# Optimization experiments

Measured on AMD Instinct MI355X. Metric: run time of the kernel, lower is better.

Reference implementation:

```python
import jax, jax.numpy as jnp
import numpy as np

N, DIN, H, OUT = 2048, 128, 64, 7


def setup_inputs() -> dict:
    key = jax.random.key(0)
    ks = jax.random.split(key, 24)

    def lin(k, out_d, in_d):
        kw, kb = jax.random.split(k)
        s = 1.0 / np.sqrt(in_d)
        W = jax.random.uniform(kw, (out_d, in_d), minval=-s, maxval=s, dtype=jnp.float32)
        b = jax.random.uniform(kb, (out_d,), minval=-s, maxval=s, dtype=jnp.float32)
        return W, b

    x = jax.random.normal(ks[0], (N, DIN), dtype=jnp.float32)
    A = jax.random.uniform(ks[1], (N, N), dtype=jnp.float32)
    W1, b1 = lin(ks[2], H, DIN)
    WF1, bF1 = lin(ks[3], H, H)
    WF2, bF2 = lin(ks[4], H, H)
    WT1, bT1 = lin(ks[5], H, H)
    WT2, bT2 = lin(ks[6], H, H)
    WC1, bC1 = lin(ks[7], H, H)
    WC2, bC2 = lin(ks[8], H, H)
    Wa, ba = lin(ks[9], H, H)
    q = jax.random.normal(ks[10], (H,), dtype=jnp.float32)
    W2, b2 = lin(ks[11], OUT, H)
    return dict(x=x, A=A, k=4, W1=W1, b1=b1, WF1=WF1, bF1=bF1, WF2=WF2, bF2=bF2,
                WT1=WT1, bT1=bT1, WT2=WT2, bT2=bT2, WC1=WC1, bC1=bC1, WC2=WC2,
                bC2=bC2, Wa=Wa, ba=ba, q=q, W2=W2, b2=b2)


def leaky(x):
    return jnp.where(x > 0, x, 0.1 * x)


def laplacian(A):
    # D^{-1/2} A D^{-1/2} with diagonal D of (rowsum + 1e-10)
    d = (jnp.sum(A, -1) + 1e-10) ** -0.5
    return A * d[:, None] * d[None, :]


def cos_sim(x):
    n = jnp.sqrt(jnp.sum(x * x, -1, keepdims=True))
    s = x / n + 1e-10  # note: +1e-10 AFTER the division, as in the source
    return s @ s.T


def heat(x):
    # exp(-0.5 * sum_d ((x_i - x_j)^2 + 1e-10)); gram trick, same math as
    # the [d, N, N] broadcasted version in the source.
    sq = jnp.sum(x * x, -1)
    dist = sq[:, None] + sq[None, :] - 2.0 * (x @ x.T) + x.shape[-1] * 1e-10
    return jnp.exp(-0.5 * dist)


def l2_norm_rows(x):
    m = jnp.sqrt(jnp.mean(x * x, -1)) + 1e-10
    return x / m[:, None]


def hsic(x1, x2):
    n = x1.shape[-2]
    K1 = x1 @ x1.T
    K2 = x2 @ x2.T
    Rm = jnp.eye(n, dtype=x1.dtype) - jnp.ones((n, n), dtype=x1.dtype) / n
    P = Rm @ K1 @ Rm  # [N, N]
    # mean(I * (P @ K2)) * n^2/(n-1)^2 = trace(P @ K2)/(n-1)^2; K2 symmetric
    return jnp.sum(P * K2) / (n - 1) ** 2


def gnn(z, Ad, W, b):
    return leaky((Ad @ z) @ W.T + b)


def reference(x, A, k, W1, b1, WF1, bF1, WF2, bF2, WT1, bT1, WT2, bT2,
              WC1, bC1, WC2, bC2, Wa, ba, q, W2, b2):
    h = leaky(x @ W1.T + b1)                       # [N, H]
    At = laplacian(A)
    Hh = heat(h)                                    # [N, N]
    rank = jnp.argsort(jnp.argsort(-Hh, axis=-1), axis=-1)  # double-argsort rank
    mask = (rank < k).astype(h.dtype)
    Af = laplacian(cos_sim(h) * mask)
    zf = gnn(gnn(h, Af, WF1, bF1), Af, WF2, bF2)
    zt = gnn(gnn(h, At, WT1, bT1), At, WT2, bT2)
    zcf = gnn(gnn(h, Af, WC1, bC1), Af, WC2, bC2)
    zct = gnn(gnn(h, At, WC1, bC1), At, WC2, bC2)
    Lcf = l2_norm_rows(zcf)
    Lct = l2_norm_rows(zct)
    Lc = jnp.mean((Lcf @ Lcf.T - Lct @ Lct.T) ** 2)
    Ld = hsic(zt, zct) + hsic(zf, zcf)
    zc = (zcf + zct) / 2
    z = jnp.stack([zf, zt, zc], axis=-2)            # [N, 3, H]
    a = jax.nn.softmax(jnp.tanh(z @ Wa.T + ba) @ q, axis=-1)  # [N, 3]
    zagg = jnp.einsum('nkd,nk->nd', z, a)           # [N, H]
    out = zagg @ W2.T + b2                          # [N, OUT]
    return (out, Lc, Ld)
```

## Files before the change

kernel.cpp:

```cpp
#include <hip/hip_runtime.h>
#include <stdint.h>

#define N 2048
#define DIN 128
#define H 64
#define OUTD 7
#define RS 32
#define S1 8
#define S2 8

#define Z_ZT  0
#define Z_ZCT 64
#define Z_ZF  128
#define Z_ZCF 192
#define Z_LCF 256
#define Z_LCT 320

typedef short bf16x8 __attribute__((ext_vector_type(8)));
typedef float floatx4 __attribute__((ext_vector_type(4)));

__device__ __forceinline__ float leaky(float x){ return x > 0.f ? x : 0.1f*x; }

__device__ __forceinline__ unsigned short f2bf(float f){
  unsigned int u = __float_as_uint(f);
  u = u + 0x7FFFu + ((u >> 16) & 1u);
  return (unsigned short)(u >> 16);
}

__device__ __forceinline__ float bf2f(unsigned short u){
  return __uint_as_float((unsigned int)u << 16);
}

__device__ __forceinline__ float waveRedSum(float v){
  #pragma unroll
  for (int o = 32; o > 0; o >>= 1) v += __shfl_xor(v, o, 64);
  return v;
}

__device__ __forceinline__ unsigned long long shflx64(unsigned long long v, int m){
  unsigned int lo = (unsigned int)v, hi = (unsigned int)(v >> 32);
  lo = (unsigned int)__shfl_xor((int)lo, m, 64);
  hi = (unsigned int)__shfl_xor((int)hi, m, 64);
  return ((unsigned long long)hi << 32) | lo;
}

__global__ void k_prep(const float* __restrict__ A, float* __restrict__ dA,
                       unsigned short* __restrict__ Abf){
  int i = blockIdx.x;
  const float4* row = (const float4*)(A + (size_t)i * N);
  unsigned short* ob = Abf + (size_t)i * N;
  float s = 0.f;
  #pragma unroll
  for (int it = 0; it < 2; it++){
    int u = threadIdx.x + it*256;
    float4 v = row[u];
    s += v.x + v.y + v.z + v.w;
    ushort4 o;
    o.x = f2bf(v.x); o.y = f2bf(v.y); o.z = f2bf(v.z); o.w = f2bf(v.w);
    *(ushort4*)&ob[u*4] = o;
  }
  __shared__ float red[4];
  s = waveRedSum(s);
  int wid = threadIdx.x >> 6, lane = threadIdx.x & 63;
  if (lane == 0) red[wid] = s;
  __syncthreads();
  if (threadIdx.x == 0){
    float t = red[0] + red[1] + red[2] + red[3];
    dA[i] = 1.0f / sqrtf(t + 1e-10f);
  }
}

__global__ __launch_bounds__(256) void k_h(const float* __restrict__ x,
                    const float* __restrict__ W1g, const float* __restrict__ b1,
                    const float* __restrict__ dA,
                    unsigned short* __restrict__ hb_hi,
                    unsigned short* __restrict__ hb_lo,
                    unsigned short* __restrict__ hsT,
                    float* __restrict__ sq, float* __restrict__ hsum){
  __shared__ float W1t[DIN][H+1];
  __shared__ float xb[4][DIN];
  __shared__ __align__(16) unsigned short hTb[H][16];
  int tid = threadIdx.x, w = tid >> 6, t = tid & 63;
  int i0 = blockIdx.x * 16;
  for (int u = tid; u < 2048; u += 256){
    float4 g = ((const float4*)W1g)[u];
    int row = u >> 5, c0 = (u & 31) * 4;
    W1t[c0+0][row] = g.x; W1t[c0+1][row] = g.y;
    W1t[c0+2][row] = g.z; W1t[c0+3][row] = g.w;
  }
  __syncthreads();
  float bt = b1[t];
  for (int rr = 0; rr < 4; rr++){
    int i = i0 + w*4 + rr;
    xb[w][t]      = x[(size_t)i*DIN + t];
    xb[w][t + 64] = x[(size_t)i*DIN + t + 64];
    float acc = bt;
    #pragma unroll
    for (int c4 = 0; c4 < DIN/4; c4++){
      float xv[4]; *(float4*)xv = *(const float4*)&xb[w][c4*4];
      acc += xv[0]*W1t[c4*4+0][t] + xv[1]*W1t[c4*4+1][t]
           + xv[2]*W1t[c4*4+2][t] + xv[3]*W1t[c4*4+3][t];
    }
    float hv = leaky(acc);
    unsigned short hi = f2bf(hv);
    hb_hi[(size_t)i*H + t] = hi;
    hb_lo[(size_t)i*H + t] = f2bf(hv - bf2f(hi));
    hTb[t][w*4+rr] = f2bf(dA[i]*hv);
    float s2 = waveRedSum(hv*hv);
    float s1 = waveRedSum(hv);
    if (t == 0){ sq[i] = s2; hsum[i] = s1; }
  }
  __syncthreads();
  { int c = tid >> 2, qq = tid & 3;
    ushort4 v = *(ushort4*)&hTb[c][qq*4];
    *(ushort4*)&hsT[(size_t)c*N + i0 + qq*4] = v; }
}

__global__ __launch_bounds__(256) void k_gram2(
    const unsigned short* __restrict__ Hhi, const unsigned short* __restrict__ Hlo,
    float* __restrict__ DOT){
  __shared__ __align__(16) unsigned short Bh[128][72];
  __shared__ __align__(16) unsigned short Bl[128][72];
  int bi = blockIdx.x, bj = blockIdx.y, tid = threadIdx.x;
  for (int u = tid; u < 1024; u += 256){
    int r = u >> 3, s = u & 7;
    *(uint4*)&Bh[r][s*8] = *(const uint4*)(Hhi + (size_t)(bj*128+r)*H + s*8);
    *(uint4*)&Bl[r][s*8] = *(const uint4*)(Hlo + (size_t)(bj*128+r)*H + s*8);
  }
  __syncthreads();
  int w = tid >> 6, lane = tid & 63, quad = lane >> 4, ml = lane & 15;
  floatx4 acc[2][8];
  #pragma unroll
  for (int rt = 0; rt < 2; rt++)
    #pragma unroll
    for (int ct = 0; ct < 8; ct++) acc[rt][ct] = (floatx4){0.f,0.f,0.f,0.f};
  #pragma unroll
  for (int rt = 0; rt < 2; rt++){
    int arow = bi*128 + (2*w + rt)*16 + ml;
    #pragma unroll
    for (int k0 = 0; k0 < 64; k0 += 32){
      bf16x8 ah = *(const bf16x8*)(Hhi + (size_t)arow*H + k0 + quad*8);
      bf16x8 al = *(const bf16x8*)(Hlo + (size_t)arow*H + k0 + quad*8);
      #pragma unroll
      for (int ct = 0; ct < 8; ct++){
        bf16x8 bh = *(const bf16x8*)&Bh[ct*16 + ml][k0 + quad*8];
        bf16x8 bl = *(const bf16x8*)&Bl[ct*16 + ml][k0 + quad*8];
        acc[rt][ct] = __builtin_amdgcn_mfma_f32_16x16x32_bf16(ah, bh, acc[rt][ct], 0,0,0);
        acc[rt][ct] = __builtin_amdgcn_mfma_f32_16x16x32_bf16(ah, bl, acc[rt][ct], 0,0,0);
        acc[rt][ct] = __builtin_amdgcn_mfma_f32_16x16x32_bf16(al, bh, acc[rt][ct], 0,0,0);
      }
    }
  }
  #pragma unroll
  for (int rt = 0; rt < 2; rt++)
    #pragma unroll
    for (int ct = 0; ct < 8; ct++)
      #pragma unroll
      for (int r = 0; r < 4; r++){
        int row = bi*128 + (2*w+rt)*16 + quad*4 + r;
        DOT[(size_t)row*N + bj*128 + ct*16 + ml] = acc[rt][ct][r];
      }
}

__global__ __launch_bounds__(256) void k_topk(const float* __restrict__ DOT,
      const float* __restrict__ sq, const float* __restrict__ hsum,
      int* __restrict__ nidx, float* __restrict__ ncos, float* __restrict__ df){
  int tid = threadIdx.x, w = tid >> 6, lane = tid & 63;
  int i = blockIdx.x*4 + w;
  const float4* row = (const float4*)(DOT + (size_t)i * N);
  const float4* sq4 = (const float4*)sq;
  unsigned long long best[4] = {~0ULL, ~0ULL, ~0ULL, ~0ULL};
  #pragma unroll
  for (int it = 0; it < 8; it++){
    int u = it*64 + lane;
    float4 d = row[u];
    float4 s = sq4[u];
    float kv[4] = { s.x - 2.f*d.x, s.y - 2.f*d.y, s.z - 2.f*d.z, s.w - 2.f*d.w };
    #pragma unroll
    for (int e = 0; e < 4; e++){
      unsigned int j = (unsigned int)(u*4 + e);
      unsigned int uk = __float_as_uint(kv[e]);
      uk = (uk & 0x80000000u) ? ~uk : (uk | 0x80000000u);
      unsigned long long c = ((unsigned long long)uk << 32) | j;
      if (c < best[3]){
        best[3] = c;
        unsigned long long t0;
        if (best[3] < best[2]){ t0 = best[2]; best[2] = best[3]; best[3] = t0; }
        if (best[2] < best[1]){ t0 = best[1]; best[1] = best[2]; best[2] = t0; }
        if (best[1] < best[0]){ t0 = best[0]; best[0] = best[1]; best[1] = t0; }
      }
    }
  }
  unsigned long long win[4];
  #pragma unroll
  for (int r = 0; r < 4; r++){
    unsigned long long m = best[0];
    #pragma unroll
    for (int o = 1; o < 64; o <<= 1){
      unsigned long long other = shflx64(m, o);
      if (other < m) m = other;
    }
    win[r] = m;
    if      (best[0]==m){best[0]=best[1];best[1]=best[2];best[2]=best[3];best[3]=~0ULL;}
    else if (best[1]==m){best[1]=best[2];best[2]=best[3];best[3]=~0ULL;}
    else if (best[2]==m){best[2]=best[3];best[3]=~0ULL;}
    else if (best[3]==m){best[3]=~0ULL;}
  }
  float myc = 0.f;
  if (lane < 4){
    unsigned long long wv = win[lane];
    unsigned int j = (unsigned int)wv;
    unsigned int uk = (unsigned int)(wv >> 32);
    float key = (uk & 0x80000000u) ? __uint_as_float(uk ^ 0x80000000u)
                                   : __uint_as_float(~uk);
    float sqj = sq[j];
    float dot = (sqj - key) * 0.5f;
    float hni = sqrtf(sq[i]), hnj = sqrtf(sqj);
    float cosv = dot/(hni*hnj)
               + 1e-10f*(hsum[i]/hni + hsum[j]/hnj)
               + 64.0f*1e-20f;
    nidx[i*4 + lane] = (int)j;
    ncos[i*4 + lane] = cosv;
    myc = cosv;
  }
  myc += __shfl_xor(myc, 1, 64);
  myc += __shfl_xor(myc, 2, 64);
  if (lane == 0) df[i] = 1.f / sqrtf(myc + 1e-10f);
}

template<int BN>
__global__ __launch_bounds__(256) void k_mgemm(
    const unsigned short* __restrict__ Abf, const unsigned short* __restrict__ BtG,
    float* __restrict__ Cp, int KC){
  __shared__ __align__(16) unsigned short Asl[64][72];
  __shared__ __align__(16) unsigned short Bsl[BN][72];
  int m0 = blockIdx.x * 64, kbase = blockIdx.y * KC;
  int tid = threadIdx.x;
  int w = tid >> 6, lane = tid & 63;
  int quad = lane >> 4, ml = lane & 15;
  floatx4 acc[BN/16];
  #pragma unroll
  for (int ct = 0; ct < BN/16; ct++) acc[ct] = (floatx4){0.f,0.f,0.f,0.f};

  for (int kc = 0; kc < KC; kc += 64){
    int kb = kbase + kc;
    #pragma unroll
    for (int u = tid; u < 512; u += 256){
      int r = u >> 3, s = u & 7;
      *(uint4*)&Asl[r][s*8] = *(const uint4*)(Abf + ((size_t)(m0+r) << 11) + kb + s*8);
    }
    #pragma unroll
    for (int u = tid; u < BN*8; u += 256){
      int n = u >> 3, s = u & 7;
      *(uint4*)&Bsl[n][s*8] = *(const uint4*)(BtG + ((size_t)n << 11) + kb + s*8);
    }
    __syncthreads();
    #pragma unroll
    for (int k0 = 0; k0 < 64; k0 += 32){
      bf16x8 af = *(const bf16x8*)&Asl[16*w + ml][k0 + quad*8];
      #pragma unroll
// ... 178 lines not shown
      bf16x8 bfr = *(const bf16x8*)&Ws[16*ct + ml][k0 + quad*8];
      acc[ct] = __builtin_amdgcn_mfma_f32_16x16x32_bf16(af, bfr, acc[ct], 0, 0, 0);
    }
  }
  int zoff = (p == 0) ? Z_ZF : (p == 1) ? Z_ZCF : (p == 2) ? Z_ZT : Z_ZCT;
  float val[4][4];
  #pragma unroll
  for (int ct = 0; ct < 4; ct++){
    int col = 16*ct + ml;
    #pragma unroll
    for (int r = 0; r < 4; r++){
      val[ct][r] = leaky(acc[ct][r] + bias[col]);
      int row = 16*w + quad*4 + r;
      Z6[(size_t)(i0+row)*384 + zoff + col] = val[ct][r];
    }
  }
  if (p == 1 || p == 3){
    int loff = (p == 1) ? Z_LCF : Z_LCT;
    #pragma unroll
    for (int r = 0; r < 4; r++){
      float s = val[0][r]*val[0][r] + val[1][r]*val[1][r]
              + val[2][r]*val[2][r] + val[3][r]*val[3][r];
      s += __shfl_xor(s, 1, 64); s += __shfl_xor(s, 2, 64);
      s += __shfl_xor(s, 4, 64); s += __shfl_xor(s, 8, 64);
      float m = sqrtf(s*(1.f/64.f)) + 1e-10f;
      int row = 16*w + quad*4 + r;
      #pragma unroll
      for (int ct = 0; ct < 4; ct++)
        Z6[(size_t)(i0+row)*384 + loff + 16*ct + ml] = val[ct][r]/m;
    }
  }
}

__global__ __launch_bounds__(256) void k_att(const float* __restrict__ Z6,
    const float* __restrict__ Wag, const float* __restrict__ ba,
    const float* __restrict__ q, const float* __restrict__ W2g,
    const float* __restrict__ b2, float* __restrict__ out){
  __shared__ float Wal[64][65];
  __shared__ float W2l[448];
  __shared__ float zbuf[4][3][66];
  __shared__ float zagg[4][66];
  int tid = threadIdx.x, w = tid >> 6, t = tid & 63;
  for (int u = tid; u < 1024; u += 256){
    int r = u >> 4, c4 = (u & 15)*4;
    float4 f = ((const float4*)Wag)[u];
    Wal[r][c4+0]=f.x; Wal[r][c4+1]=f.y; Wal[r][c4+2]=f.z; Wal[r][c4+3]=f.w;
  }
  if (tid < 112) *(float4*)&W2l[tid*4] = ((const float4*)W2g)[tid];
  __syncthreads();
  int i = blockIdx.x*4 + w;
  const float* zr = Z6 + (size_t)i*384;
  float zf = zr[Z_ZF + t], zt = zr[Z_ZT + t];
  float zc = 0.5f*(zr[Z_ZCF + t] + zr[Z_ZCT + t]);
  zbuf[w][0][t] = zf; zbuf[w][1][t] = zt; zbuf[w][2][t] = zc;
  __syncthreads();
  float bav = ba[t], qv = q[t];
  float e[3];
  #pragma unroll
  for (int k = 0; k < 3; k++){
    float S = bav;
    #pragma unroll 8
    for (int c = 0; c < 64; c++) S += zbuf[w][k][c] * Wal[t][c];
    e[k] = waveRedSum(tanhf(S)*qv);
  }
  float mx = fmaxf(e[0], fmaxf(e[1], e[2]));
  float x0 = expf(e[0]-mx), x1 = expf(e[1]-mx), x2 = expf(e[2]-mx);
  float inv = 1.f/(x0+x1+x2);
  zagg[w][t] = x0*inv*zf + x1*inv*zt + x2*inv*zc;
  __syncthreads();
  if (t < OUTD){
    float acc = b2[t];
    #pragma unroll 8
    for (int c = 0; c < 64; c++) acc += zagg[w][c]*W2l[t*64 + c];
    out[(size_t)i*OUTD + t] = acc;
  }
}

__global__ __launch_bounds__(256) void k_reduce(const float* __restrict__ Z6,
                                                float* __restrict__ redP,
                                                float* __restrict__ colP){
  __shared__ float sa[64][68];
  __shared__ float sb[64][68];
  int p = blockIdx.x >> 5;
  int s = blockIdx.x & 31;
  int tid = threadIdx.x;
  const int aoffT[5] = {Z_ZT,  Z_ZF,  Z_LCF, Z_LCF, Z_LCT};
  const int boffT[5] = {Z_ZCT, Z_ZCF, Z_LCF, Z_LCT, Z_LCT};
  int aoff = aoffT[p], boff = boffT[p];
  int r0 = s * 64;
  {
    int row = tid >> 4, c4 = (tid & 15) * 4;
    #pragma unroll
    for (int rr = 0; rr < 64; rr += 16){
      const float* zr = Z6 + (size_t)(r0 + row + rr) * 384;
      *(float4*)&sa[row + rr][c4] = *(const float4*)&zr[aoff + c4];
      *(float4*)&sb[row + rr][c4] = *(const float4*)&zr[boff + c4];
    }
  }
  __syncthreads();
  int rg = tid >> 4, cg = tid & 15;
  float acc[4][4] = {};
  #pragma unroll 8
  for (int k = 0; k < 64; k++){
    float a[4], b[4];
    *(float4*)a = *(const float4*)&sa[k][rg*4];
    *(float4*)b = *(const float4*)&sb[k][cg*4];
    #pragma unroll
    for (int ii = 0; ii < 4; ii++)
      #pragma unroll
      for (int jj = 0; jj < 4; jj++)
        acc[ii][jj] += a[ii]*b[jj];
  }
  float* rp = redP + (size_t)blockIdx.x * 4096;
  #pragma unroll
  for (int ii = 0; ii < 4; ii++)
    *(float4*)&rp[(rg*4+ii)*64 + cg*4] =
      make_float4(acc[ii][0], acc[ii][1], acc[ii][2], acc[ii][3]);
  if (p < 2 && tid < 128){
    int t = tid & 63;
    float csum = 0.f;
    if (tid < 64){
      #pragma unroll 16
      for (int r = 0; r < 64; r++) csum += sa[r][t];
    } else {
      #pragma unroll 16
      for (int r = 0; r < 64; r++) csum += sb[r][t];
    }
    colP[((size_t)p*RS + s)*128 + tid] = csum;
  }
}

__global__ void k_combine(const float* __restrict__ redP,
                          const float* __restrict__ colP,
                          float* __restrict__ red){
  int idx = blockIdx.x*256 + threadIdx.x;
  if (idx < 20480){
    int p = idx >> 12, i = idx & 4095;
    float sum = 0.f;
    #pragma unroll 8
    for (int s = 0; s < RS; s++) sum += redP[((size_t)p*RS + s)*4096 + i];
    red[idx] = sum;
  } else if (idx < 20736){
    int j = idx - 20480;
    int p = j >> 7, rem = j & 127;
    float sum = 0.f;
    #pragma unroll 8
    for (int s = 0; s < RS; s++) sum += colP[((size_t)p*RS + s)*128 + rem];
    red[idx] = sum;
  }
}

__global__ void k_final(const float* __restrict__ red, float* __restrict__ out2){
  int tid = threadIdx.x;
  const float* Stc = red;
  const float* Sfc = red + 4096;
  const float* Cff = red + 8192;
  const float* Cft = red + 12288;
  const float* Ctt = red + 16384;
  const float* cst = red + 20480;
  const float* csct= red + 20544;
  const float* csf = red + 20608;
// ... 28 lines not shown
                              void* d_out, int out_size, void* d_ws, size_t ws_size,
                              hipStream_t stream) {
  const float* x   = (const float*)d_in[0];
  const float* A   = (const float*)d_in[1];
  const float* W1  = (const float*)d_in[3];
  const float* b1  = (const float*)d_in[4];
  const float* WF1 = (const float*)d_in[5];
  const float* bF1 = (const float*)d_in[6];
  const float* WF2 = (const float*)d_in[7];
  const float* bF2 = (const float*)d_in[8];
  const float* WT1 = (const float*)d_in[9];
  const float* bT1 = (const float*)d_in[10];
  const float* WT2 = (const float*)d_in[11];
  const float* bT2 = (const float*)d_in[12];
  const float* WC1 = (const float*)d_in[13];
  const float* bC1 = (const float*)d_in[14];
  const float* WC2 = (const float*)d_in[15];
  const float* bC2 = (const float*)d_in[16];
  const float* Wa  = (const float*)d_in[17];
  const float* ba  = (const float*)d_in[18];
  const float* q   = (const float*)d_in[19];
  const float* W2  = (const float*)d_in[20];
  const float* b2  = (const float*)d_in[21];
  float* out = (float*)d_out;

  float* W = (float*)d_ws;
  float* dA   = W;
  float* sq   = dA  + N;
  float* hsum = sq  + N;
  float* df   = hsum+ N;
  int*   nidx = (int*)(df + N);
  float* ncos = (float*)(nidx + N*4);
  float* red  = ncos + N*4;
  float* DOT  = red + 20736;
  float* Z6   = DOT + (size_t)N*N;
  float* Y1p  = Z6  + (size_t)N*384;
  float* Y2p  = Y1p + (size_t)S1*N*H;
  float* z1f  = Y2p + (size_t)S2*N*128;
  float* z1cf = z1f + N*H;
  float* redP = z1cf+ N*H;
  float* colP = redP+ 655360;
  unsigned short* Abf  = (unsigned short*)(colP + 8192);
  unsigned short* hsT  = Abf + (size_t)N*N;
  unsigned short* ZsT  = hsT + (size_t)H*N;
  unsigned short* hbHi = ZsT + (size_t)128*N;
  unsigned short* hbLo = hbHi + (size_t)N*H;

  k_prep<<<N, 256, 0, stream>>>(A, dA, Abf);
  k_h<<<128, 256, 0, stream>>>(x, W1, b1, dA, hbHi, hbLo, hsT, sq, hsum);
  k_gram2<<<dim3(16,16), 256, 0, stream>>>(hbHi, hbLo, DOT);
  k_topk<<<512, 256, 0, stream>>>(DOT, sq, hsum, nidx, ncos, df);

  k_mgemm<64><<<dim3(32,S1), 256, 0, stream>>>(Abf, hsT, Y1p, N/S1);
  k_z1m<<<dim3(32,4), 256, 0, stream>>>(hbHi, nidx, ncos, df, Y1p, dA,
                                        WF1, WC1, WT1, bF1, bC1, bT1,
                                        z1f, z1cf, ZsT);
  k_mgemm<128><<<dim3(32,S2), 256, 0, stream>>>(Abf, ZsT, Y2p, N/S2);
  k_z2m<<<dim3(32,4), 256, 0, stream>>>(z1f, z1cf, nidx, ncos, df, Y2p, dA,
                                        WF2, WC2, WT2, bF2, bC2, bT2, Z6);
  k_att<<<512, 256, 0, stream>>>(Z6, Wa, ba, q, W2, b2, out);
  k_reduce<<<5*RS, 256, 0, stream>>>(Z6, redP, colP);
  k_combine<<<81, 256, 0, stream>>>(redP, colP, red);
  k_final<<<1, 256, 0, stream>>>(red, out + (size_t)N*OUTD);
}
```

Baseline: 197.2 us.

## Fuse gram with top-k selection, merge prep into h, and merge attention with reduce

The heat-kernel gram matrix is no longer written to a 16 MB DOT buffer and re-read by a separate top-k kernel. Top-k is now selected in registers right after each MFMA tile, with per-row candidates merged by 16-lane shuffles. The A row-sum/bf16 conversion is folded into the h kernel, which cuts the grid from 2048 blocks to 128. The attention and reduce kernels are merged into one launch. Together these remove launches and a large global round trip, but gramtop now runs on only 32 blocks, which leaves most CUs idle, and the prep work runs on far fewer blocks.

```diff
diff --git a/kernel.cpp b/kernel.cpp
--- a/kernel.cpp
+++ b/kernel.cpp
@@ -44,35 +44,10 @@
   return ((unsigned long long)hi << 32) | lo;
 }
 
-__global__ void k_prep(const float* __restrict__ A, float* __restrict__ dA,
-                       unsigned short* __restrict__ Abf){
-  int i = blockIdx.x;
-  const float4* row = (const float4*)(A + (size_t)i * N);
-  unsigned short* ob = Abf + (size_t)i * N;
-  float s = 0.f;
-  #pragma unroll
-  for (int it = 0; it < 2; it++){
-    int u = threadIdx.x + it*256;
-    float4 v = row[u];
-    s += v.x + v.y + v.z + v.w;
-    ushort4 o;
-    o.x = f2bf(v.x); o.y = f2bf(v.y); o.z = f2bf(v.z); o.w = f2bf(v.w);
-    *(ushort4*)&ob[u*4] = o;
-  }
-  __shared__ float red[4];
-  s = waveRedSum(s);
-  int wid = threadIdx.x >> 6, lane = threadIdx.x & 63;
-  if (lane == 0) red[wid] = s;
-  __syncthreads();
-  if (threadIdx.x == 0){
-    float t = red[0] + red[1] + red[2] + red[3];
-    dA[i] = 1.0f / sqrtf(t + 1e-10f);
-  }
-}
-
-__global__ __launch_bounds__(256) void k_h(const float* __restrict__ x,
+__global__ __launch_bounds__(256) void k_preph(const float* __restrict__ A,
+                    const float* __restrict__ x,
                     const float* __restrict__ W1g, const float* __restrict__ b1,
-                    const float* __restrict__ dA,
+                    float* __restrict__ dA, unsigned short* __restrict__ Abf,
                     unsigned short* __restrict__ hb_hi,
                     unsigned short* __restrict__ hb_lo,
                     unsigned short* __restrict__ hsT,
@@ -80,7 +55,8 @@
   __shared__ float W1t[DIN][H+1];
   __shared__ float xb[4][DIN];
   __shared__ __align__(16) unsigned short hTb[H][16];
-  int tid = threadIdx.x, w = tid >> 6, t = tid & 63;
+  __shared__ float dAl[16];
+  int tid = threadIdx.x, w = tid >> 6, lane = tid & 63;
   int i0 = blockIdx.x * 16;
   for (int u = tid; u < 2048; u += 256){
     float4 g = ((const float4*)W1g)[u];
@@ -88,7 +64,28 @@
     W1t[c0+0][row] = g.x; W1t[c0+1][row] = g.y;
     W1t[c0+2][row] = g.z; W1t[c0+3][row] = g.w;
   }
+  for (int rr = 0; rr < 4; rr++){
+    int i = i0 + w*4 + rr;
+    const float4* row = (const float4*)(A + (size_t)i * N);
+    unsigned short* ob = Abf + (size_t)i * N;
+    float s = 0.f;
+    #pragma unroll
+    for (int it = 0; it < 8; it++){
+      int u = it*64 + lane;
+      float4 v = row[u];
+      s += v.x + v.y + v.z + v.w;
+      ushort4 o;
+      o.x = f2bf(v.x); o.y = f2bf(v.y); o.z = f2bf(v.z); o.w = f2bf(v.w);
+      *(ushort4*)&ob[u*4] = o;
+    }
+    s = waveRedSum(s);
+    if (lane == 0){
+      float d = 1.0f / sqrtf(s + 1e-10f);
+      dA[i] = d; dAl[w*4+rr] = d;
+    }
+  }
   __syncthreads();
+  int t = lane;
   float bt = b1[t];
   for (int rr = 0; rr < 4; rr++){
     int i = i0 + w*4 + rr;
@@ -105,7 +102,7 @@
     unsigned short hi = f2bf(hv);
     hb_hi[(size_t)i*H + t] = hi;
     hb_lo[(size_t)i*H + t] = f2bf(hv - bf2f(hi));
-    hTb[t][w*4+rr] = f2bf(dA[i]*hv);
+    hTb[t][w*4+rr] = f2bf(dAl[w*4+rr]*hv);
     float s2 = waveRedSum(hv*hv);
     float s1 = waveRedSum(hv);
     if (t == 0){ sq[i] = s2; hsum[i] = s1; }
@@ -116,116 +113,107 @@
     *(ushort4*)&hsT[(size_t)c*N + i0 + qq*4] = v; }
 }
 
-__global__ __launch_bounds__(256) void k_gram2(
+__global__ __launch_bounds__(256) void k_gramtop(
     const unsigned short* __restrict__ Hhi, const unsigned short* __restrict__ Hlo,
-    float* __restrict__ DOT){
+    const float* __restrict__ sq, const float* __restrict__ hsum,
+    int* __restrict__ nidx, float* __restrict__ ncos, float* __restrict__ df){
   __shared__ __align__(16) unsigned short Bh[128][72];
   __shared__ __align__(16) unsigned short Bl[128][72];
-  int bi = blockIdx.x, bj = blockIdx.y, tid = threadIdx.x;
-  for (int u = tid; u < 1024; u += 256){
-    int r = u >> 3, s = u & 7;
-    *(uint4*)&Bh[r][s*8] = *(const uint4*)(Hhi + (size_t)(bj*128+r)*H + s*8);
-    *(uint4*)&Bl[r][s*8] = *(const uint4*)(Hlo + (size_t)(bj*128+r)*H + s*8);
-  }
-  __syncthreads();
-  int w = tid >> 6, lane = tid & 63, quad = lane >> 4, ml = lane & 15;
-  floatx4 acc[2][8];
-  #pragma unroll
-  for (int rt = 0; rt < 2; rt++)
-    #pragma unroll
-    for (int ct = 0; ct < 8; ct++) acc[rt][ct] = (floatx4){0.f,0.f,0.f,0.f};
-  #pragma unroll
-  for (int rt = 0; rt < 2; rt++){
-    int arow = bi*128 + (2*w + rt)*16 + ml;
-    #pragma unroll
-    for (int k0 = 0; k0 < 64; k0 += 32){
-      bf16x8 ah = *(const bf16x8*)(Hhi + (size_t)arow*H + k0 + quad*8);
-      bf16x8 al = *(const bf16x8*)(Hlo + (size_t)arow*H + k0 + quad*8);
-      #pragma unroll
-      for (int ct = 0; ct < 8; ct++){
-        bf16x8 bh = *(const bf16x8*)&Bh[ct*16 + ml][k0 + quad*8];
-        bf16x8 bl = *(const bf16x8*)&Bl[ct*16 + ml][k0 + quad*8];
-        acc[rt][ct] = __builtin_amdgcn_mfma_f32_16x16x32_bf16(ah, bh, acc[rt][ct], 0,0,0);
-        acc[rt][ct] = __builtin_amdgcn_mfma_f32_16x16x32_bf16(ah, bl, acc[rt][ct], 0,0,0);
-        acc[rt][ct] = __builtin_amdgcn_mfma_f32_16x16x32_bf16(al, bh, acc[rt][ct], 0,0,0);
-      }
-    }
-  }
-  #pragma unroll
-  for (int rt = 0; rt < 2; rt++)
-    #pragma unroll
-    for (int ct = 0; ct < 8; ct++)
+  __shared__ float sqs[2048];
+  int tid = threadIdx.x, w = tid >> 6, lane = tid & 63;
+  int quad = lane >> 4, ml = lane & 15;
+  int i0 = blockIdx.x * 64;
+  for (int u = tid; u < 512; u += 256)
+    ((float4*)sqs)[u] = ((const float4*)sq)[u];
+  int arow = i0 + w*16 + ml;
+  bf16x8 ah0 = *(const bf16x8*)(Hhi + (size_t)arow*H + quad*8);
+  bf16x8 ah1 = *(const bf16x8*)(Hhi + (size_t)arow*H + 32 + quad*8);
+  bf16x8 al0 = *(const bf16x8*)(Hlo + (size_t)arow*H + quad*8);
+  bf16x8 al1 = *(const bf16x8*)(Hlo + (size_t)arow*H + 32 + quad*8);
+  unsigned long long best[4][4];
+  #pragma unroll
+  for (int r = 0; r < 4; r++)
+    #pragma unroll
+    for (int e = 0; e < 4; e++) best[r][e] = ~0ULL;
+
+  for (int cb = 0; cb < 16; cb++){
+    int c0 = cb * 128;
+    __syncthreads();
+    for (int u = tid; u < 1024; u += 256){
+      int r = u >> 3, s = u & 7;
+      *(uint4*)&Bh[r][s*8] = *(const uint4*)(Hhi + (size_t)(c0+r)*H + s*8);
+      *(uint4*)&Bl[r][s*8] = *(const uint4*)(Hlo + (size_t)(c0+r)*H + s*8);
+    }
+    __syncthreads();
+    #pragma unroll
+    for (int ct = 0; ct < 8; ct++){
+      floatx4 acc = (floatx4){0.f,0.f,0.f,0.f};
+      bf16x8 bh0 = *(const bf16x8*)&Bh[ct*16+ml][quad*8];
+      bf16x8 bh1 = *(const bf16x8*)&Bh[ct*16+ml][32+quad*8];
+      bf16x8 bl0 = *(const bf16x8*)&Bl[ct*16+ml][quad*8];
+      bf16x8 bl1 = *(const bf16x8*)&Bl[ct*16+ml][32+quad*8];
+      acc = __builtin_amdgcn_mfma_f32_16x16x32_bf16(ah0, bh0, acc, 0,0,0);
+      acc = __builtin_amdgcn_mfma_f32_16x16x32_bf16(ah1, bh1, acc, 0,0,0);
+      acc = __builtin_amdgcn_mfma_f32_16x16x32_bf16(ah0, bl0, acc, 0,0,0);
+      acc = __builtin_amdgcn_mfma_f32_16x16x32_bf16(ah1, bl1, acc, 0,0,0);
+      acc = __builtin_amdgcn_mfma_f32_16x16x32_bf16(al0, bh0, acc, 0,0,0);
+      acc = __builtin_amdgcn_mfma_f32_16x16x32_bf16(al1, bh1, acc, 0,0,0);
+      unsigned int col = (unsigned int)(c0 + ct*16 + ml);
+      float sqc = sqs[col];
       #pragma unroll
       for (int r = 0; r < 4; r++){
-        int row = bi*128 + (2*w+rt)*16 + quad*4 + r;
-        DOT[(size_t)row*N + bj*128 + ct*16 + ml] = acc[rt][ct][r];
-      }
-}
-
-__global__ __launch_bounds__(256) void k_topk(const float* __restrict__ DOT,
-      const float* __restrict__ sq, const float* __restrict__ hsum,
-      int* __restrict__ nidx, float* __restrict__ ncos, float* __restrict__ df){
-  int tid = threadIdx.x, w = tid >> 6, lane = tid & 63;
-  int i = blockIdx.x*4 + w;
-  const float4* row = (const float4*)(DOT + (size_t)i * N);
-  const float4* sq4 = (const float4*)sq;
-  unsigned long long best[4] = {~0ULL, ~0ULL, ~0ULL, ~0ULL};
-  #pragma unroll
-  for (int it = 0; it < 8; it++){
-    int u = it*64 + lane;
-    float4 d = row[u];
-    float4 s = sq4[u];
-    float kv[4] = { s.x - 2.f*d.x, s.y - 2.f*d.y, s.z - 2.f*d.z, s.w - 2.f*d.w };
+        float kv = sqc - 2.f*acc[r];
+        unsigned int uk = __float_as_uint(kv);
+        uk = (uk & 0x80000000u) ? ~uk : (uk | 0x80000000u);
+        unsigned long long cc = ((unsigned long long)uk << 32) | col;
+        if (cc < best[r][3]){
+          best[r][3] = cc;
+          unsigned long long t0;
+          if (best[r][3] < best[r][2]){ t0=best[r][2]; best[r][2]=best[r][3]; best[r][3]=t0; }
+          if (best[r][2] < best[r][1]){ t0=best[r][1]; best[r][1]=best[r][2]; best[r][2]=t0; }
+          if (best[r][1] < best[r][0]){ t0=best[r][0]; best[r][0]=best[r][1]; best[r][1]=t0; }
+        }
+      }
+    }
+  }
+  #pragma unroll
+  for (int r = 0; r < 4; r++){
+    unsigned long long w0=~0ULL, w1=~0ULL, w2=~0ULL, w3=~0ULL;
     #pragma unroll
     for (int e = 0; e < 4; e++){
-      unsigned int j = (unsigned int)(u*4 + e);
-      unsigned int uk = __float_as_uint(kv[e]);
-      uk = (uk & 0x80000000u) ? ~uk : (uk | 0x80000000u);
-      unsigned long long c = ((unsigned long long)uk << 32) | j;
-      if (c < best[3]){
-        best[3] = c;
-        unsigned long long t0;
-        if (best[3] < best[2]){ t0 = best[2]; best[2] = best[3]; best[3] = t0; }
-        if (best[2] < best[1]){ t0 = best[1]; best[1] = best[2]; best[2] = t0; }
-        if (best[1] < best[0]){ t0 = best[0]; best[0] = best[1]; best[1] = t0; }
-      }
-    }
-  }
-  unsigned long long win[4];
-  #pragma unroll
-  for (int r = 0; r < 4; r++){
-    unsigned long long m = best[0];
-    #pragma unroll
-    for (int o = 1; o < 64; o <<= 1){
-      unsigned long long other = shflx64(m, o);
-      if (other < m) m = other;
-    }
-    win[r] = m;
-    if      (best[0]==m){best[0]=best[1];best[1]=best[2];best[2]=best[3];best[3]=~0ULL;}
-    else if (best[1]==m){best[1]=best[2];best[2]=best[3];best[3]=~0ULL;}
-    else if (best[2]==m){best[2]=best[3];best[3]=~0ULL;}
-    else if (best[3]==m){best[3]=~0ULL;}
-  }
-  float myc = 0.f;
-  if (lane < 4){
-    unsigned long long wv = win[lane];
-    unsigned int j = (unsigned int)wv;
-    unsigned int uk = (unsigned int)(wv >> 32);
-    float key = (uk & 0x80000000u) ? __uint_as_float(uk ^ 0x80000000u)
-                                   : __uint_as_float(~uk);
-    float sqj = sq[j];
-    float dot = (sqj - key) * 0.5f;
-    float hni = sqrtf(sq[i]), hnj = sqrtf(sqj);
-    float cosv = dot/(hni*hnj)
-               + 1e-10f*(hsum[i]/hni + hsum[j]/hnj)
-               + 64.0f*1e-20f;
-    nidx[i*4 + lane] = (int)j;
-    ncos[i*4 + lane] = cosv;
-    myc = cosv;
-  }
-  myc += __shfl_xor(myc, 1, 64);
-  myc += __shfl_xor(myc, 2, 64);
-  if (lane == 0) df[i] = 1.f / sqrtf(myc + 1e-10f);
+      unsigned long long m = best[r][0];
+      unsigned long long o1 = shflx64(m, 1); if (o1 < m) m = o1;
+      unsigned long long o2 = shflx64(m, 2); if (o2 < m) m = o2;
+      unsigned long long o4 = shflx64(m, 4); if (o4 < m) m = o4;
+      unsigned long long o8 = shflx64(m, 8); if (o8 < m) m = o8;
+      if (e == 0) w0 = m; else if (e == 1) w1 = m; else if (e == 2) w2 = m; else w3 = m;
+      if      (best[r][0]==m){best[r][0]=best[r][1];best[r][1]=best[r][2];best[r][2]=best[r][3];best[r][3]=~0ULL;}
+      else if (best[r][1]==m){best[r][1]=best[r][2];best[r][2]=best[r][3];best[r][3]=~0ULL;}
+      else if (best[r][2]==m){best[r][2]=best[r][3];best[r][3]=~0ULL;}
+      else if (best[r][3]==m){best[r][3]=~0ULL;}
+    }
+    int rowi = i0 + w*16 + quad*4 + r;
+    float myc = 0.f;
+    if (ml < 4){
+      unsigned long long wv = (ml==0)?w0:(ml==1)?w1:(ml==2)?w2:w3;
+      unsigned int j = (unsigned int)wv;
+      unsigned int uk = (unsigned int)(wv >> 32);
+      float key = (uk & 0x80000000u) ? __uint_as_float(uk ^ 0x80000000u)
+                                     : __uint_as_float(~uk);
+      float sqj = sqs[j];
+      float dot = (sqj - key) * 0.5f;
+      float hni = sqrtf(sqs[rowi]), hnj = sqrtf(sqj);
+      float cosv = dot/(hni*hnj)
+                 + 1e-10f*(hsum[rowi]/hni + hsum[j]/hnj)
+                 + 64.0f*1e-20f;
+      nidx[rowi*4 + ml] = (int)j;
+      ncos[rowi*4 + ml] = cosv;
+      myc = cosv;
+    }
+    myc += __shfl_xor(myc, 1, 64);
+    myc += __shfl_xor(myc, 2, 64);
+    if (ml == 0) df[rowi] = 1.f / sqrtf(myc + 1e-10f);
+  }
 }
 
 template<int BN>
@@ -470,101 +458,99 @@
   }
 }
 
-__global__ __launch_bounds__(256) void k_att(const float* __restrict__ Z6,
+__global__ __launch_bounds__(256) void k_attred(const float* __restrict__ Z6,
     const float* __restrict__ Wag, const float* __restrict__ ba,
     const float* __restrict__ q, const float* __restrict__ W2g,
-    const float* __restrict__ b2, float* __restrict__ out){
+    const float* __restrict__ b2, float* __restrict__ out,
+    float* __restrict__ redP, float* __restrict__ colP){
   __shared__ float Wal[64][65];
   __shared__ float W2l[448];
   __shared__ float zbuf[4][3][66];
   __shared__ float zagg[4][66];
-  int tid = threadIdx.x, w = tid >> 6, t = tid & 63;
-  for (int u = tid; u < 1024; u += 256){
-    int r = u >> 4, c4 = (u & 15)*4;
-    float4 f = ((const float4*)Wag)[u];
-    Wal[r][c4+0]=f.x; Wal[r][c4+1]=f.y; Wal[r][c4+2]=f.z; Wal[r][c4+3]=f.w;
-  }
-  if (tid < 112) *(float4*)&W2l[tid*4] = ((const float4*)W2g)[tid];
-  __syncthreads();
-  int i = blockIdx.x*4 + w;
-  const float* zr = Z6 + (size_t)i*384;
-  float zf = zr[Z_ZF + t], zt = zr[Z_ZT + t];
-  float zc = 0.5f*(zr[Z_ZCF + t] + zr[Z_ZCT + t]);
-  zbuf[w][0][t] = zf; zbuf[w][1][t] = zt; zbuf[w][2][t] = zc;
-  __syncthreads();
-  float bav = ba[t], qv = q[t];
-  float e[3];
-  #pragma unroll
-  for (int k = 0; k < 3; k++){
-    float S = bav;
-    #pragma unroll 8
-    for (int c = 0; c < 64; c++) S += zbuf[w][k][c] * Wal[t][c];
-    e[k] = waveRedSum(tanhf(S)*qv);
-  }
-  float mx = fmaxf(e[0], fmaxf(e[1], e[2]));
-  float x0 = expf(e[0]-mx), x1 = expf(e[1]-mx), x2 = expf(e[2]-mx);
-  float inv = 1.f/(x0+x1+x2);
-  zagg[w][t] = x0*inv*zf + x1*inv*zt + x2*inv*zc;
-  __syncthreads();
-  if (t < OUTD){
-    float acc = b2[t];
-    #pragma unroll 8
-    for (int c = 0; c < 64; c++) acc += zagg[w][c]*W2l[t*64 + c];
-    out[(size_t)i*OUTD + t] = acc;
-  }
-}
-
-__global__ __launch_bounds__(256) void k_reduce(const float* __restrict__ Z6,
-                                                float* __restrict__ redP,
-                                                float* __restrict__ colP){
   __shared__ float sa[64][68];
   __shared__ float sb[64][68];
-  int p = blockIdx.x >> 5;
-  int s = blockIdx.x & 31;
-  int tid = threadIdx.x;
-  const int aoffT[5] = {Z_ZT,  Z_ZF,  Z_LCF, Z_LCF, Z_LCT};
-  const int boffT[5] = {Z_ZCT, Z_ZCF, Z_LCF, Z_LCT, Z_LCT};
-  int aoff = aoffT[p], boff = boffT[p];
-  int r0 = s * 64;
-  {
-    int row = tid >> 4, c4 = (tid & 15) * 4;
-    #pragma unroll
-    for (int rr = 0; rr < 64; rr += 16){
-      const float* zr = Z6 + (size_t)(r0 + row + rr) * 384;
-      *(float4*)&sa[row + rr][c4] = *(const float4*)&zr[aoff + c4];
-      *(float4*)&sb[row + rr][c4] = *(const float4*)&zr[boff + c4];
-    }
-  }
-  __syncthreads();
-  int rg = tid >> 4, cg = tid & 15;
-  float acc[4][4] = {};
-  #pragma unroll 8
-  for (int k = 0; k < 64; k++){
-    float a[4], b[4];
-    *(float4*)a = *(const float4*)&sa[k][rg*4];
-    *(float4*)b = *(const float4*)&sb[k][cg*4];
+  int tid = threadIdx.x, w = tid >> 6, t = tid & 63;
+  if (blockIdx.x < 512){
+    for (int u = tid; u < 1024; u += 256){
+      int r = u >> 4, c4 = (u & 15)*4;
+      float4 f = ((const float4*)Wag)[u];
+      Wal[r][c4+0]=f.x; Wal[r][c4+1]=f.y; Wal[r][c4+2]=f.z; Wal[r][c4+3]=f.w;
+    }
+    if (tid < 112) *(float4*)&W2l[tid*4] = ((const float4*)W2g)[tid];
+    __syncthreads();
+    int i = blockIdx.x*4 + w;
+    const float* zr = Z6 + (size_t)i*384;
+    float zf = zr[Z_ZF + t], zt = zr[Z_ZT + t];
+    float zc = 0.5f*(zr[Z_ZCF + t] + zr[Z_ZCT + t]);
+    zbuf[w][0][t] = zf; zbuf[w][1][t] = zt; zbuf[w][2][t] = zc;
+    __syncthreads();
+    float bav = ba[t], qv = q[t];
+    float e[3];
+    #pragma unroll
+    for (int k = 0; k < 3; k++){
+      float S = bav;
+      #pragma unroll 8
+      for (int c = 0; c < 64; c++) S += zbuf[w][k][c] * Wal[t][c];
+      e[k] = waveRedSum(tanhf(S)*qv);
+    }
+    float mx = fmaxf(e[0], fmaxf(e[1], e[2]));
+    float x0 = expf(e[0]-mx), x1 = expf(e[1]-mx), x2 = expf(e[2]-mx);
+    float inv = 1.f/(x0+x1+x2);
+    zagg[w][t] = x0*inv*zf + x1*inv*zt + x2*inv*zc;
+    __syncthreads();
+    if (t < OUTD){
+      float acc = b2[t];
+      #pragma unroll 8
+      for (int c = 0; c < 64; c++) acc += zagg[w][c]*W2l[t*64 + c];
+      out[(size_t)i*OUTD + t] = acc;
+    }
+  } else {
+    int bb = blockIdx.x - 512;
+    int p = bb >> 5, s = bb & 31;
+    const int aoffT[5] = {Z_ZT,  Z_ZF,  Z_LCF, Z_LCF, Z_LCT};
+    const int boffT[5] = {Z_ZCT, Z_ZCF, Z_LCF, Z_LCT, Z_LCT};
+    int aoff = aoffT[p], boff = boffT[p];
+    int r0 = s * 64;
+    {
+      int row = tid >> 4, c4 = (tid & 15) * 4;
+      #pragma unroll
+      for (int rr = 0; rr < 64; rr += 16){
+        const float* zr = Z6 + (size_t)(r0 + row + rr) * 384;
+        *(float4*)&sa[row + rr][c4] = *(const float4*)&zr[aoff + c4];
+        *(float4*)&sb[row + rr][c4] = *(const float4*)&zr[boff + c4];
+      }
+    }
+    __syncthreads();
+    int rg = tid >> 4, cg = tid & 15;
+    float acc[4][4] = {};
+    #pragma unroll 8
+    for (int k = 0; k < 64; k++){
+      float a[4], b[4];
+      *(float4*)a = *(const float4*)&sa[k][rg*4];
+      *(float4*)b = *(const float4*)&sb[k][cg*4];
+      #pragma unroll
+      for (int ii = 0; ii < 4; ii++)
+        #pragma unroll
+        for (int jj = 0; jj < 4; jj++)
+          acc[ii][jj] += a[ii]*b[jj];
+    }
+    float* rp = redP + (size_t)bb * 4096;
     #pragma unroll
     for (int ii = 0; ii < 4; ii++)
-      #pragma unroll
-      for (int jj = 0; jj < 4; jj++)
-        acc[ii][jj] += a[ii]*b[jj];
-  }
-  float* rp = redP + (size_t)blockIdx.x * 4096;
-  #pragma unroll
-  for (int ii = 0; ii < 4; ii++)
-    *(float4*)&rp[(rg*4+ii)*64 + cg*4] =
-      make_float4(acc[ii][0], acc[ii][1], acc[ii][2], acc[ii][3]);
-  if (p < 2 && tid < 128){
-    int t = tid & 63;
-    float csum = 0.f;
-    if (tid < 64){
-      #pragma unroll 16
-      for (int r = 0; r < 64; r++) csum += sa[r][t];
-    } else {
-      #pragma unroll 16
-      for (int r = 0; r < 64; r++) csum += sb[r][t];
-    }
-    colP[((size_t)p*RS + s)*128 + tid] = csum;
+      *(float4*)&rp[(rg*4+ii)*64 + cg*4] =
+        make_float4(acc[ii][0], acc[ii][1], acc[ii][2], acc[ii][3]);
+    if (p < 2 && tid < 128){
+      int tt = tid & 63;
+      float csum = 0.f;
+      if (tid < 64){
+        #pragma unroll 16
+        for (int r = 0; r < 64; r++) csum += sa[r][tt];
+      } else {
+        #pragma unroll 16
+        for (int r = 0; r < 64; r++) csum += sb[r][tt];
+      }
+      colP[((size_t)p*RS + s)*128 + tid] = csum;
+    }
   }
 }
 
@@ -659,8 +645,7 @@
   int*   nidx = (int*)(df + N);
   float* ncos = (float*)(nidx + N*4);
   float* red  = ncos + N*4;
-  float* DOT  = red + 20736;
-  float* Z6   = DOT + (size_t)N*N;
+  float* Z6   = red + 20736;
   float* Y1p  = Z6  + (size_t)N*384;
   float* Y2p  = Y1p + (size_t)S1*N*H;
   float* z1f  = Y2p + (size_t)S2*N*128;
@@ -673,11 +658,8 @@
   unsigned short* hbHi = ZsT + (size_t)128*N;
   unsigned short* hbLo = hbHi + (size_t)N*H;
 
-  k_prep<<<N, 256, 0, stream>>>(A, dA, Abf);
-  k_h<<<128, 256, 0, stream>>>(x, W1, b1, dA, hbHi, hbLo, hsT, sq, hsum);
-  k_gram2<<<dim3(16,16), 256, 0, stream>>>(hbHi, hbLo, DOT);
-  k_topk<<<512, 256, 0, stream>>>(DOT, sq, hsum, nidx, ncos, df);
-
+  k_preph<<<128, 256, 0, stream>>>(A, x, W1, b1, dA, Abf, hbHi, hbLo, hsT, sq, hsum);
+  k_gramtop<<<32, 256, 0, stream>>>(hbHi, hbLo, sq, hsum, nidx, ncos, df);
   k_mgemm<64><<<dim3(32,S1), 256, 0, stream>>>(Abf, hsT, Y1p, N/S1);
   k_z1m<<<dim3(32,4), 256, 0, stream>>>(hbHi, nidx, ncos, df, Y1p, dA,
                                         WF1, WC1, WT1, bF1, bC1, bT1,
@@ -685,8 +667,7 @@
   k_mgemm<128><<<dim3(32,S2), 256, 0, stream>>>(Abf, ZsT, Y2p, N/S2);
   k_z2m<<<dim3(32,4), 256, 0, stream>>>(z1f, z1cf, nidx, ncos, df, Y2p, dA,
                                         WF2, WC2, WT2, bF2, bC2, bT2, Z6);
-  k_att<<<512, 256, 0, stream>>>(Z6, Wa, ba, q, W2, b2, out);
-  k_reduce<<<5*RS, 256, 0, stream>>>(Z6, redP, colP);
+  k_attred<<<672, 256, 0, stream>>>(Z6, Wa, ba, q, W2, b2, out, redP, colP);
   k_combine<<<81, 256, 0, stream>>>(redP, colP, red);
   k_final<<<1, 256, 0, stream>>>(red, out + (size_t)N*OUTD);
 }
```

New measurement: 257.6 us. 1.31x slower.

## Fuse A preprocessing into h kernel and merge attention with reduction kernel

Applied to the files above, without the earlier changes.

The adjacency row-sum and bf16 conversion move into the kernel computing h, so each block handles 16 rows of A and keeps its inverse degree in shared memory. The attention/output kernel and the Gram reduction kernel become one launch, with blocks chosen by index. This removes two kernel launches and the dA round trip through global memory. In exchange, A conversion runs on far fewer blocks, which may underuse memory bandwidth, and the merged kernel carries more shared memory, which may lower occupancy.

```diff
diff --git a/kernel.cpp b/kernel.cpp
--- a/kernel.cpp
+++ b/kernel.cpp
@@ -44,35 +44,10 @@
   return ((unsigned long long)hi << 32) | lo;
 }
 
-__global__ void k_prep(const float* __restrict__ A, float* __restrict__ dA,
-                       unsigned short* __restrict__ Abf){
-  int i = blockIdx.x;
-  const float4* row = (const float4*)(A + (size_t)i * N);
-  unsigned short* ob = Abf + (size_t)i * N;
-  float s = 0.f;
-  #pragma unroll
-  for (int it = 0; it < 2; it++){
-    int u = threadIdx.x + it*256;
-    float4 v = row[u];
-    s += v.x + v.y + v.z + v.w;
-    ushort4 o;
-    o.x = f2bf(v.x); o.y = f2bf(v.y); o.z = f2bf(v.z); o.w = f2bf(v.w);
-    *(ushort4*)&ob[u*4] = o;
-  }
-  __shared__ float red[4];
-  s = waveRedSum(s);
-  int wid = threadIdx.x >> 6, lane = threadIdx.x & 63;
-  if (lane == 0) red[wid] = s;
-  __syncthreads();
-  if (threadIdx.x == 0){
-    float t = red[0] + red[1] + red[2] + red[3];
-    dA[i] = 1.0f / sqrtf(t + 1e-10f);
-  }
-}
-
-__global__ __launch_bounds__(256) void k_h(const float* __restrict__ x,
+__global__ __launch_bounds__(256) void k_preph(const float* __restrict__ A,
+                    const float* __restrict__ x,
                     const float* __restrict__ W1g, const float* __restrict__ b1,
-                    const float* __restrict__ dA,
+                    float* __restrict__ dA, unsigned short* __restrict__ Abf,
                     unsigned short* __restrict__ hb_hi,
                     unsigned short* __restrict__ hb_lo,
                     unsigned short* __restrict__ hsT,
@@ -80,7 +55,8 @@
   __shared__ float W1t[DIN][H+1];
   __shared__ float xb[4][DIN];
   __shared__ __align__(16) unsigned short hTb[H][16];
-  int tid = threadIdx.x, w = tid >> 6, t = tid & 63;
+  __shared__ float dAl[16];
+  int tid = threadIdx.x, w = tid >> 6, lane = tid & 63;
   int i0 = blockIdx.x * 16;
   for (int u = tid; u < 2048; u += 256){
     float4 g = ((const float4*)W1g)[u];
@@ -88,7 +64,28 @@
     W1t[c0+0][row] = g.x; W1t[c0+1][row] = g.y;
     W1t[c0+2][row] = g.z; W1t[c0+3][row] = g.w;
   }
+  for (int rr = 0; rr < 4; rr++){
+    int i = i0 + w*4 + rr;
+    const float4* row = (const float4*)(A + (size_t)i * N);
+    unsigned short* ob = Abf + (size_t)i * N;
+    float s = 0.f;
+    #pragma unroll
+    for (int it = 0; it < 8; it++){
+      int u = it*64 + lane;
+      float4 v = row[u];
+      s += v.x + v.y + v.z + v.w;
+      ushort4 o;
+      o.x = f2bf(v.x); o.y = f2bf(v.y); o.z = f2bf(v.z); o.w = f2bf(v.w);
+      *(ushort4*)&ob[u*4] = o;
+    }
+    s = waveRedSum(s);
+    if (lane == 0){
+      float d = 1.0f / sqrtf(s + 1e-10f);
+      dA[i] = d; dAl[w*4+rr] = d;
+    }
+  }
   __syncthreads();
+  int t = lane;
   float bt = b1[t];
   for (int rr = 0; rr < 4; rr++){
     int i = i0 + w*4 + rr;
@@ -105,7 +102,7 @@
     unsigned short hi = f2bf(hv);
     hb_hi[(size_t)i*H + t] = hi;
     hb_lo[(size_t)i*H + t] = f2bf(hv - bf2f(hi));
-    hTb[t][w*4+rr] = f2bf(dA[i]*hv);
+    hTb[t][w*4+rr] = f2bf(dAl[w*4+rr]*hv);
     float s2 = waveRedSum(hv*hv);
     float s1 = waveRedSum(hv);
     if (t == 0){ sq[i] = s2; hsum[i] = s1; }
@@ -470,101 +467,99 @@
   }
 }
 
-__global__ __launch_bounds__(256) void k_att(const float* __restrict__ Z6,
+__global__ __launch_bounds__(256) void k_attred(const float* __restrict__ Z6,
     const float* __restrict__ Wag, const float* __restrict__ ba,
     const float* __restrict__ q, const float* __restrict__ W2g,
-    const float* __restrict__ b2, float* __restrict__ out){
+    const float* __restrict__ b2, float* __restrict__ out,
+    float* __restrict__ redP, float* __restrict__ colP){
   __shared__ float Wal[64][65];
   __shared__ float W2l[448];
   __shared__ float zbuf[4][3][66];
   __shared__ float zagg[4][66];
-  int tid = threadIdx.x, w = tid >> 6, t = tid & 63;
-  for (int u = tid; u < 1024; u += 256){
-    int r = u >> 4, c4 = (u & 15)*4;
-    float4 f = ((const float4*)Wag)[u];
-    Wal[r][c4+0]=f.x; Wal[r][c4+1]=f.y; Wal[r][c4+2]=f.z; Wal[r][c4+3]=f.w;
-  }
-  if (tid < 112) *(float4*)&W2l[tid*4] = ((const float4*)W2g)[tid];
-  __syncthreads();
-  int i = blockIdx.x*4 + w;
-  const float* zr = Z6 + (size_t)i*384;
-  float zf = zr[Z_ZF + t], zt = zr[Z_ZT + t];
-  float zc = 0.5f*(zr[Z_ZCF + t] + zr[Z_ZCT + t]);
-  zbuf[w][0][t] = zf; zbuf[w][1][t] = zt; zbuf[w][2][t] = zc;
-  __syncthreads();
-  float bav = ba[t], qv = q[t];
-  float e[3];
-  #pragma unroll
-  for (int k = 0; k < 3; k++){
-    float S = bav;
-    #pragma unroll 8
-    for (int c = 0; c < 64; c++) S += zbuf[w][k][c] * Wal[t][c];
-    e[k] = waveRedSum(tanhf(S)*qv);
-  }
-  float mx = fmaxf(e[0], fmaxf(e[1], e[2]));
-  float x0 = expf(e[0]-mx), x1 = expf(e[1]-mx), x2 = expf(e[2]-mx);
-  float inv = 1.f/(x0+x1+x2);
-  zagg[w][t] = x0*inv*zf + x1*inv*zt + x2*inv*zc;
-  __syncthreads();
-  if (t < OUTD){
-    float acc = b2[t];
-    #pragma unroll 8
-    for (int c = 0; c < 64; c++) acc += zagg[w][c]*W2l[t*64 + c];
-    out[(size_t)i*OUTD + t] = acc;
-  }
-}
-
-__global__ __launch_bounds__(256) void k_reduce(const float* __restrict__ Z6,
-                                                float* __restrict__ redP,
-                                                float* __restrict__ colP){
   __shared__ float sa[64][68];
   __shared__ float sb[64][68];
-  int p = blockIdx.x >> 5;
-  int s = blockIdx.x & 31;
-  int tid = threadIdx.x;
-  const int aoffT[5] = {Z_ZT,  Z_ZF,  Z_LCF, Z_LCF, Z_LCT};
-  const int boffT[5] = {Z_ZCT, Z_ZCF, Z_LCF, Z_LCT, Z_LCT};
-  int aoff = aoffT[p], boff = boffT[p];
-  int r0 = s * 64;
-  {
-    int row = tid >> 4, c4 = (tid & 15) * 4;
-    #pragma unroll
-    for (int rr = 0; rr < 64; rr += 16){
-      const float* zr = Z6 + (size_t)(r0 + row + rr) * 384;
-      *(float4*)&sa[row + rr][c4] = *(const float4*)&zr[aoff + c4];
-      *(float4*)&sb[row + rr][c4] = *(const float4*)&zr[boff + c4];
-    }
-  }
-  __syncthreads();
-  int rg = tid >> 4, cg = tid & 15;
-  float acc[4][4] = {};
-  #pragma unroll 8
-  for (int k = 0; k < 64; k++){
-    float a[4], b[4];
-    *(float4*)a = *(const float4*)&sa[k][rg*4];
-    *(float4*)b = *(const float4*)&sb[k][cg*4];
+  int tid = threadIdx.x, w = tid >> 6, t = tid & 63;
+  if (blockIdx.x < 512){
+    for (int u = tid; u < 1024; u += 256){
+      int r = u >> 4, c4 = (u & 15)*4;
+      float4 f = ((const float4*)Wag)[u];
+      Wal[r][c4+0]=f.x; Wal[r][c4+1]=f.y; Wal[r][c4+2]=f.z; Wal[r][c4+3]=f.w;
+    }
+    if (tid < 112) *(float4*)&W2l[tid*4] = ((const float4*)W2g)[tid];
+    __syncthreads();
+    int i = blockIdx.x*4 + w;
+    const float* zr = Z6 + (size_t)i*384;
+    float zf = zr[Z_ZF + t], zt = zr[Z_ZT + t];
+    float zc = 0.5f*(zr[Z_ZCF + t] + zr[Z_ZCT + t]);
+    zbuf[w][0][t] = zf; zbuf[w][1][t] = zt; zbuf[w][2][t] = zc;
+    __syncthreads();
+    float bav = ba[t], qv = q[t];
+    float e[3];
+    #pragma unroll
+    for (int k = 0; k < 3; k++){
+      float S = bav;
+      #pragma unroll 8
+      for (int c = 0; c < 64; c++) S += zbuf[w][k][c] * Wal[t][c];
+      e[k] = waveRedSum(tanhf(S)*qv);
+    }
+    float mx = fmaxf(e[0], fmaxf(e[1], e[2]));
+    float x0 = expf(e[0]-mx), x1 = expf(e[1]-mx), x2 = expf(e[2]-mx);
+    float inv = 1.f/(x0+x1+x2);
+    zagg[w][t] = x0*inv*zf + x1*inv*zt + x2*inv*zc;
+    __syncthreads();
+    if (t < OUTD){
+      float acc = b2[t];
+      #pragma unroll 8
+      for (int c = 0; c < 64; c++) acc += zagg[w][c]*W2l[t*64 + c];
+      out[(size_t)i*OUTD + t] = acc;
+    }
+  } else {
+    int bb = blockIdx.x - 512;
+    int p = bb >> 5, s = bb & 31;
+    const int aoffT[5] = {Z_ZT,  Z_ZF,  Z_LCF, Z_LCF, Z_LCT};
+    const int boffT[5] = {Z_ZCT, Z_ZCF, Z_LCF, Z_LCT, Z_LCT};
+    int aoff = aoffT[p], boff = boffT[p];
+    int r0 = s * 64;
+    {
+      int row = tid >> 4, c4 = (tid & 15) * 4;
+      #pragma unroll
+      for (int rr = 0; rr < 64; rr += 16){
+        const float* zr = Z6 + (size_t)(r0 + row + rr) * 384;
+        *(float4*)&sa[row + rr][c4] = *(const float4*)&zr[aoff + c4];
+        *(float4*)&sb[row + rr][c4] = *(const float4*)&zr[boff + c4];
+      }
+    }
+    __syncthreads();
+    int rg = tid >> 4, cg = tid & 15;
+    float acc[4][4] = {};
+    #pragma unroll 8
+    for (int k = 0; k < 64; k++){
+      float a[4], b[4];
+      *(float4*)a = *(const float4*)&sa[k][rg*4];
+      *(float4*)b = *(const float4*)&sb[k][cg*4];
+      #pragma unroll
+      for (int ii = 0; ii < 4; ii++)
+        #pragma unroll
+        for (int jj = 0; jj < 4; jj++)
+          acc[ii][jj] += a[ii]*b[jj];
+    }
+    float* rp = redP + (size_t)bb * 4096;
     #pragma unroll
     for (int ii = 0; ii < 4; ii++)
-      #pragma unroll
-      for (int jj = 0; jj < 4; jj++)
-        acc[ii][jj] += a[ii]*b[jj];
-  }
-  float* rp = redP + (size_t)blockIdx.x * 4096;
-  #pragma unroll
-  for (int ii = 0; ii < 4; ii++)
-    *(float4*)&rp[(rg*4+ii)*64 + cg*4] =
-      make_float4(acc[ii][0], acc[ii][1], acc[ii][2], acc[ii][3]);
-  if (p < 2 && tid < 128){
-    int t = tid & 63;
-    float csum = 0.f;
-    if (tid < 64){
-      #pragma unroll 16
-      for (int r = 0; r < 64; r++) csum += sa[r][t];
-    } else {
-      #pragma unroll 16
-      for (int r = 0; r < 64; r++) csum += sb[r][t];
-    }
-    colP[((size_t)p*RS + s)*128 + tid] = csum;
+      *(float4*)&rp[(rg*4+ii)*64 + cg*4] =
+        make_float4(acc[ii][0], acc[ii][1], acc[ii][2], acc[ii][3]);
+    if (p < 2 && tid < 128){
+      int tt = tid & 63;
+      float csum = 0.f;
+      if (tid < 64){
+        #pragma unroll 16
+        for (int r = 0; r < 64; r++) csum += sa[r][tt];
+      } else {
+        #pragma unroll 16
+        for (int r = 0; r < 64; r++) csum += sb[r][tt];
+      }
+      colP[((size_t)p*RS + s)*128 + tid] = csum;
+    }
   }
 }
 
@@ -673,11 +668,9 @@
   unsigned short* hbHi = ZsT + (size_t)128*N;
   unsigned short* hbLo = hbHi + (size_t)N*H;
 
-  k_prep<<<N, 256, 0, stream>>>(A, dA, Abf);
-  k_h<<<128, 256, 0, stream>>>(x, W1, b1, dA, hbHi, hbLo, hsT, sq, hsum);
+  k_preph<<<128, 256, 0, stream>>>(A, x, W1, b1, dA, Abf, hbHi, hbLo, hsT, sq, hsum);
   k_gram2<<<dim3(16,16), 256, 0, stream>>>(hbHi, hbLo, DOT);
   k_topk<<<512, 256, 0, stream>>>(DOT, sq, hsum, nidx, ncos, df);
-
   k_mgemm<64><<<dim3(32,S1), 256, 0, stream>>>(Abf, hsT, Y1p, N/S1);
   k_z1m<<<dim3(32,4), 256, 0, stream>>>(hbHi, nidx, ncos, df, Y1p, dA,
                                         WF1, WC1, WT1, bF1, bC1, bT1,
@@ -685,8 +678,7 @@
   k_mgemm<128><<<dim3(32,S2), 256, 0, stream>>>(Abf, ZsT, Y2p, N/S2);
   k_z2m<<<dim3(32,4), 256, 0, stream>>>(z1f, z1cf, nidx, ncos, df, Y2p, dA,
                                         WF2, WC2, WT2, bF2, bC2, bT2, Z6);
-  k_att<<<512, 256, 0, stream>>>(Z6, Wa, ba, q, W2, b2, out);
-  k_reduce<<<5*RS, 256, 0, stream>>>(Z6, redP, colP);
+  k_attred<<<672, 256, 0, stream>>>(Z6, Wa, ba, q, W2, b2, out, redP, colP);
   k_combine<<<81, 256, 0, stream>>>(redP, colP, red);
   k_final<<<1, 256, 0, stream>>>(red, out + (size_t)N*OUTD);
 }
```

Result: no change. 199.3 us (+1.1%).
